# Kernel tuning notes

Measured on AMD Instinct MI355X. Metric: run time of the kernel, lower is better.

## Reference

```python
import jax, jax.numpy as jnp
import numpy as np

N_NODES = 50000
N_EDGES = 500000
NFEAT = 128
NHID = 128
NOUT = 16


def setup_inputs() -> dict:
    key = jax.random.key(0)
    ks = jax.random.split(key, 8)
    x = jax.random.normal(ks[0], (N_NODES, NFEAT), dtype=jnp.float32)
    edge_src = jax.random.randint(ks[1], (N_EDGES,), 0, N_NODES, dtype=jnp.int32)
    edge_dst = jax.random.randint(ks[2], (N_EDGES,), 0, N_NODES, dtype=jnp.int32)
    edge_weight = jax.random.uniform(ks[3], (N_EDGES,), dtype=jnp.float32)
    # Glorot-ish init for linear weights, zero bias (PyG GCNConv default bias=0)
    def glorot(k, fan_in, fan_out):
        s = jnp.sqrt(6.0 / (fan_in + fan_out))
        return jax.random.uniform(k, (fan_in, fan_out), jnp.float32, -s, s)
    W1 = glorot(ks[4], NFEAT, NHID)
    W2 = glorot(ks[5], NHID, NHID)
    W3 = glorot(ks[6], NHID, NOUT)
    b1 = jnp.zeros((NHID,), jnp.float32)
    b2 = jnp.zeros((NHID,), jnp.float32)
    b3 = jnp.zeros((NOUT,), jnp.float32)
    return {"x": x, "edge_src": edge_src, "edge_dst": edge_dst,
            "edge_weight": edge_weight, "W1": W1, "b1": b1,
            "W2": W2, "b2": b2, "W3": W3, "b3": b3}


def gcn_conv(x, src, dst, ew, W, b):
    """PyG GCNConv: symmetric-normalized aggregation with self-loops (weight 1).

    out_i = sum_{(j->i)} d_i^{-1/2} w_ji d_j^{-1/2} (x_j W) + d_i^{-1} (x_i W) + b
    where d_i = 1 + sum of incoming edge weights.
    """
    n = x.shape[0]
    xw = x @ W                                            # [N, F_out]
    deg = jax.ops.segment_sum(ew, dst, num_segments=n) + 1.0  # self-loop weight 1
    dinv = jnp.where(deg > 0, jax.lax.rsqrt(deg), 0.0)    # d^{-1/2}
    norm = dinv[src] * ew * dinv[dst]                     # [E]
    agg = jax.ops.segment_sum(xw[src] * norm[:, None], dst, num_segments=n)
    self_loop = xw * (dinv * dinv)[:, None]               # d_i^{-1} * x_i W
    return agg + self_loop + b


def reference(x, edge_src, edge_dst, edge_weight, W1, b1, W2, b2, W3, b3):
    # Dropout layers are identity in eval mode.
    h = gcn_conv(x, edge_src, edge_dst, edge_weight, W1, b1)
    h = jax.nn.relu(h)
    h = gcn_conv(h, edge_src, edge_dst, edge_weight, W2, b2)
    h = jax.nn.relu(h)
    h = gcn_conv(h, edge_src, edge_dst, edge_weight, W3, b3)
    return jax.nn.log_softmax(h, axis=1)
```

## Files before the change

### kernel.cpp

```cpp
#include <hip/hip_runtime.h>
#include <math.h>

#define NN 50000
#define NE 500000
#define NF 128
#define NO 16
#define SCAN_B 1024
#define NPART 16

typedef __attribute__((ext_vector_type(8))) _Float16 half8;


__global__ void k_count_rank(const int* __restrict__ dst, int* __restrict__ pcnt,
                             int* __restrict__ rank, int E) {
    int part = blockIdx.x & (NPART - 1);
    int e = blockIdx.x * blockDim.x + threadIdx.x;
    if (e < E) {
        int d = dst[e];
        rank[e] = atomicAdd(&pcnt[part * NN + d], 1);
    }
}

__global__ void k_combine(int* __restrict__ pcnt, int* __restrict__ counts, int N) {
    int n = blockIdx.x * blockDim.x + threadIdx.x;
    if (n < N) {
        int run = 0;
#pragma unroll
        for (int p = 0; p < NPART; ++p) {
            int v = pcnt[p * NN + n];
            pcnt[p * NN + n] = run;
            run += v;
        }
        counts[n] = run;
    }
}

__global__ void k_scan1(const int* __restrict__ counts, int* __restrict__ offs,
                        int* __restrict__ bsums, int N) {
    __shared__ int s[SCAN_B];
    int t = threadIdx.x;
    int i = blockIdx.x * SCAN_B + t;
    int c = (i < N) ? counts[i] : 0;
    s[t] = c;
    __syncthreads();
    for (int off = 1; off < SCAN_B; off <<= 1) {
        int x = (t >= off) ? s[t - off] : 0;
        __syncthreads();
        s[t] += x;
        __syncthreads();
    }
    if (i < N) offs[i] = s[t] - c;
    if (t == SCAN_B - 1) bsums[blockIdx.x] = s[t];
}

__global__ void k_scan2(int* __restrict__ bsums, int NB) {
    if (threadIdx.x == 0 && blockIdx.x == 0) {
        int run = 0;
        for (int i = 0; i < NB; ++i) { int c = bsums[i]; bsums[i] = run; run += c; }
    }
}

__global__ void k_scan3(int* __restrict__ offs, const int* __restrict__ bsums,
                        int N, int E) {
    int i = blockIdx.x * blockDim.x + threadIdx.x;
    if (i < N) {
        offs[i] = offs[i] + bsums[i >> 10];
    } else if (i == N) {
        offs[N] = E;
    }
}

__global__ void k_scatter(const int* __restrict__ src, const int* __restrict__ dst,
                          const float* __restrict__ ew, const int* __restrict__ offs,
                          const int* __restrict__ pcnt, const int* __restrict__ rank,
                          int* __restrict__ src_s, float* __restrict__ ew_s, int E) {
    int part = blockIdx.x & (NPART - 1);
    int e = blockIdx.x * blockDim.x + threadIdx.x;
    if (e < E) {
        int d = dst[e];
        int p = offs[d] + pcnt[part * NN + d] + rank[e];
        src_s[p] = src[e];
        ew_s[p]  = ew[e];
    }
}

__global__ void k_dinv_csr(const float* __restrict__ ew_s, const int* __restrict__ offs,
                           float* __restrict__ dinv, int N) {
    int n = blockIdx.x * blockDim.x + threadIdx.x;
    if (n < N) {
        float deg = 1.0f;
        int s = offs[n], e = offs[n + 1];
        for (int j = s; j < e; ++j) deg += ew_s[j];
        dinv[n] = rsqrtf(deg);
    }
}

__global__ void k_norm_csr(const float* __restrict__ ew_s, const int* __restrict__ src_s,
                           const int* __restrict__ offs, const float* __restrict__ dinv,
                           float* __restrict__ norm_s, int N) {
    int n = blockIdx.x * blockDim.x + threadIdx.x;
    if (n < N) {
        float dn = dinv[n];
        int s = offs[n], e = offs[n + 1];
        for (int j = s; j < e; ++j)
            norm_s[j] = dinv[src_s[j]] * ew_s[j] * dn;
    }
}

__global__ __launch_bounds__(256) void k_gemm128(const float* __restrict__ X,
                                                 const float* __restrict__ W,
                                                 _Float16* __restrict__ Y, int M) {
    __shared__ float Xs[64][68];
    __shared__ float Ws[64][128];
    const int tid = threadIdx.x;
    const int tx = tid & 15;
    const int ty = tid >> 4;
    const int r0g = blockIdx.x * 64;

    float acc[4][8];
#pragma unroll
    for (int i = 0; i < 4; ++i)
#pragma unroll
        for (int j = 0; j < 8; ++j) acc[i][j] = 0.0f;

    for (int kc = 0; kc < 128; kc += 64) {
        {
            int rr = tid >> 4;
            int k4 = tid & 15;
#pragma unroll
            for (int it = 0; it < 4; ++it) {
                int row = it * 16 + rr;
                int grow = r0g + row; if (grow > M - 1) grow = M - 1;
                float4 v = *(const float4*)(X + (size_t)grow * NF + kc + k4 * 4);
                *(float4*)(&Xs[row][k4 * 4]) = v;
            }
        }
        {
            int kk0 = tid >> 5;
            int c4  = tid & 31;
#pragma unroll
            for (int it = 0; it < 8; ++it) {
                int kk = it * 8 + kk0;
                float4 v = *(const float4*)(W + (size_t)(kc + kk) * NF + c4 * 4);
                *(float4*)(&Ws[kk][c4 * 4]) = v;
            }
        }
        __syncthreads();

#pragma unroll 8
        for (int k = 0; k < 64; ++k) {
            float a0 = Xs[ty * 4 + 0][k];
            float a1 = Xs[ty * 4 + 1][k];
            float a2 = Xs[ty * 4 + 2][k];
            float a3 = Xs[ty * 4 + 3][k];
            float4 b0 = *(const float4*)(&Ws[k][tx * 8]);
            float4 b1 = *(const float4*)(&Ws[k][tx * 8 + 4]);
            float bb[8] = {b0.x, b0.y, b0.z, b0.w, b1.x, b1.y, b1.z, b1.w};
#pragma unroll
            for (int j = 0; j < 8; ++j) {
                acc[0][j] = fmaf(a0, bb[j], acc[0][j]);
                acc[1][j] = fmaf(a1, bb[j], acc[1][j]);
                acc[2][j] = fmaf(a2, bb[j], acc[2][j]);
                acc[3][j] = fmaf(a3, bb[j], acc[3][j]);
            }
        }
        __syncthreads();
    }

#pragma unroll
    for (int i = 0; i < 4; ++i) {
        int row = r0g + ty * 4 + i;
        if (row < M) {
            half8 hv;
#pragma unroll
            for (int j = 0; j < 8; ++j) hv[j] = (_Float16)acc[i][j];
            *(half8*)(Y + (size_t)row * NF + tx * 8) = hv;
        }
    }
}

__global__ __launch_bounds__(256) void k_agg128h(const _Float16* __restrict__ xw,
                                                 const float* __restrict__ dinv,
                                                 const int* __restrict__ offs,
                                                 const int* __restrict__ src_s,
                                                 const float* __restrict__ norm_s,
                                                 const float* __restrict__ bias,
                                                 float* __restrict__ out, int relu) {
    const int tid = threadIdx.x;
    const int ln = tid & 63;
    int n = __builtin_amdgcn_readfirstlane(blockIdx.x * 4 + (tid >> 6));

    union CV { unsigned int u; _Float16 h[2]; };

    float di = dinv[n];
    CV sv; sv.u = *(const unsigned int*)(xw + (size_t)n * NF + ln * 2);
    float acc0 = (float)sv.h[0] * (di * di);
    float acc1 = (float)sv.h[1] * (di * di);

    int s = offs[n], e = offs[n + 1];
    int j = s;
    for (; j + 1 < e; j += 2) {
        int s0 = src_s[j], s1 = src_s[j + 1];
        float w0 = norm_s[j], w1 = norm_s[j + 1];
        CV u0, u1;
        u0.u = *(const unsigned int*)(xw + (size_t)s0 * NF + ln * 2);
        u1.u = *(const unsigned int*)(xw + (size_t)s1 * NF + ln * 2);
        acc0 = fmaf((float)u0.h[0], w0, acc0);
        acc1 = fmaf((float)u0.h[1], w0, acc1);
        acc0 = fmaf((float)u1.h[0], w1, acc0);
        acc1 = fmaf((float)u1.h[1], w1, acc1);
    }
    if (j < e) {
        int s0 = src_s[j];
        float w0 = norm_s[j];
        CV u0; u0.u = *(const unsigned int*)(xw + (size_t)s0 * NF + ln * 2);
        acc0 = fmaf((float)u0.h[0], w0, acc0);
        acc1 = fmaf((float)u0.h[1], w0, acc1);
    }
    acc0 += bias[ln * 2];
    acc1 += bias[ln * 2 + 1];
    if (relu) { acc0 = fmaxf(acc0, 0.0f); acc1 = fmaxf(acc1, 0.0f); }
    float2 o = {acc0, acc1};
    *(float2*)(out + (size_t)n * NF + ln * 2) = o;
}

__global__ __launch_bounds__(256) void k_gemm16(const float* __restrict__ H,
                                                const float* __restrict__ W3,
                                                float* __restrict__ Y, int M) {
    __shared__ float Wl[NF * NO];
    __shared__ float Hs[16 * 132];
    int tid = threadIdx.x;
    for (int i = tid; i < NF * NO; i += 256) Wl[i] = W3[i];
    int n0 = blockIdx.x * 16;
#pragma unroll
    for (int it = 0; it < 2; ++it) {
        int idx = tid + it * 256;
        int r = idx >> 5, f4 = idx & 31;
        int gr = n0 + r; if (gr > M - 1) gr = M - 1;
        *(float4*)(&Hs[r * 132 + f4 * 4]) = *(const float4*)(H + (size_t)gr * NF + f4 * 4);
    }
    __syncthreads();
    int ln = tid >> 4, c = tid & 15;
    float acc = 0.0f;
#pragma unroll 8
    for (int k = 0; k < NF; ++k) acc = fmaf(Hs[ln * 132 + k], Wl[k * NO + c], acc);
    int n = n0 + ln;
    if (n < M) Y[(size_t)n * NO + c] = acc;
}

__global__ __launch_bounds__(256) void k_agg16_ls(const float* __restrict__ xw,
                                                  const float* __restrict__ dinv,
                                                  const int* __restrict__ offs,
                                                  const int* __restrict__ src_s,
                                                  const float* __restrict__ norm_s,
                                                  const float* __restrict__ bias,
                                                  float* __restrict__ out) {
    int tid = threadIdx.x;
    int ln = tid >> 4, c = tid & 15;
    int n = blockIdx.x * 16 + ln;
    float di = dinv[n];
    float acc = xw[(size_t)n * NO + c] * (di * di);
    int s = offs[n], e = offs[n + 1];
    for (int j = s; j < e; ++j) {
        acc = fmaf(xw[(size_t)src_s[j] * NO + c], norm_s[j], acc);
    }
    acc += bias[c];
    float m = acc;
#pragma unroll
    for (int off = 8; off > 0; off >>= 1) m = fmaxf(m, __shfl_xor(m, off, 16));
    float ex = expf(acc - m);
    float ss = ex;
#pragma unroll
    for (int off = 8; off > 0; off >>= 1) ss += __shfl_xor(ss, off, 16);
    out[(size_t)n * NO + c] = acc - m - logf(ss);
}


extern "C" void kernel_launch(void* const* d_in, const int* in_sizes, int n_in,
                              void* d_out, int out_size, void* d_ws, size_t ws_size,
                              hipStream_t stream) {
    const float* x   = (const float*)d_in[0];
    const int*   esrc= (const int*)  d_in[1];
    const int*   edst= (const int*)  d_in[2];
    const float* ew  = (const float*)d_in[3];
    const float* W1  = (const float*)d_in[4];
    const float* b1  = (const float*)d_in[5];
    const float* W2  = (const float*)d_in[6];
    const float* b2  = (const float*)d_in[7];
    const float* W3  = (const float*)d_in[8];
    const float* b3  = (const float*)d_in[9];
    float* out = (float*)d_out;

    char* p = (char*)d_ws;
    _Float16* xw  = (_Float16*)p; p += (size_t)NN * NF * 2;
    float* h      = (float*)p; p += (size_t)NN * NF * 4;
    float* xw3    = (float*)p; p += (size_t)NN * NO * 4;
    float* dinv   = (float*)p; p += (size_t)NN * 4;
    float* norm_s = (float*)p; p += (size_t)NE * 4;
    int*   src_s  = (int*)p;   p += (size_t)NE * 4;
    float* ew_s   = (float*)p; p += (size_t)NE * 4;
    int*   rank   = (int*)p;   p += (size_t)NE * 4;
    int*   pcnt   = (int*)p;   p += (size_t)NPART * NN * 4;
    int*   counts = (int*)p;   p += (size_t)NN * 4;
    int*   offs   = (int*)p;   p += (size_t)(NN + 1) * 4;
    int*   bsums  = (int*)p;   p += 256;

    const int NB  = (NN + SCAN_B - 1) / SCAN_B;
    const int EBL = (NE + 255) / 256;
    const int NBL = (NN + 255) / 256;

    hipMemsetAsync(pcnt, 0, (size_t)NPART * NN * 4, stream);

    k_count_rank<<<EBL, 256, 0, stream>>>(edst, pcnt, rank, NE);
    k_combine<<<NBL, 256, 0, stream>>>(pcnt, counts, NN);
    k_scan1<<<NB, SCAN_B, 0, stream>>>(counts, offs, bsums, NN);
    k_scan2<<<1, 64, 0, stream>>>(bsums, NB);
    k_scan3<<<(NN + 256) / 256, 256, 0, stream>>>(offs, bsums, NN, NE);
    k_scatter<<<EBL, 256, 0, stream>>>(esrc, edst, ew, offs, pcnt, rank, src_s, ew_s, NE);
    k_dinv_csr<<<NBL, 256, 0, stream>>>(ew_s, offs, dinv, NN);
    k_norm_csr<<<NBL, 256, 0, stream>>>(ew_s, src_s, offs, dinv, norm_s, NN);

    k_gemm128<<<(NN + 63) / 64, 256, 0, stream>>>(x, W1, xw, NN);
    k_agg128h<<<NN / 4, 256, 0, stream>>>(xw, dinv, offs, src_s, norm_s, b1, h, 1);
    k_gemm128<<<(NN + 63) / 64, 256, 0, stream>>>(h, W2, xw, NN);
    k_agg128h<<<NN / 4, 256, 0, stream>>>(xw, dinv, offs, src_s, norm_s, b2, h, 1);
    k_gemm16<<<(NN + 15) / 16, 256, 0, stream>>>(h, W3, xw3, NN);
    k_agg16_ls<<<NN / 16, 256, 0, stream>>>(xw3, dinv, offs, src_s, norm_s, b3, out);
}
```

Before: 293.3 us.

## Use MFMA fp16 GEMMs, fold normalization into GEMM epilogue, store fp16 hidden

The scalar fp32 GEMMs are replaced by MFMA 16x16x32 fp16 kernels that read pre-transposed fp16 weights. Each kernel also pre-scales its output rows by dinv, which removes the separate per-edge norm kernel, since aggregation can then use the raw edge weights and a final dinv multiply. Hidden activations are now stored in fp16 to halve their traffic, the aggregation loop is unrolled by 4, and the block-sum scan uses a wave shuffle instead of a single thread. Lower precision in the GEMM inputs and in the hidden activations risks accuracy drift.

```diff
diff --git a/kernel.cpp b/kernel.cpp
--- a/kernel.cpp
+++ b/kernel.cpp
@@ -8,7 +8,8 @@
 #define SCAN_B 1024
 #define NPART 16
 
-typedef __attribute__((ext_vector_type(8))) _Float16 half8;
+typedef _Float16 f16x8 __attribute__((ext_vector_type(8)));
+typedef float f32x4 __attribute__((ext_vector_type(4)));
 
 
 __global__ void k_count_rank(const int* __restrict__ dst, int* __restrict__ pcnt,
@@ -54,10 +55,15 @@
 }
 
 __global__ void k_scan2(int* __restrict__ bsums, int NB) {
-    if (threadIdx.x == 0 && blockIdx.x == 0) {
-        int run = 0;
-        for (int i = 0; i < NB; ++i) { int c = bsums[i]; bsums[i] = run; run += c; }
-    }
+    int t = threadIdx.x;
+    int v = (t < NB) ? bsums[t] : 0;
+    int orig = v;
+#pragma unroll
+    for (int off = 1; off < 64; off <<= 1) {
+        int u = __shfl_up(v, off, 64);
+        if (t >= off) v += u;
+    }
+    if (t < NB) bsums[t] = v - orig;
 }
 
 __global__ void k_scan3(int* __restrict__ offs, const int* __restrict__ bsums,
@@ -95,97 +101,86 @@
     }
 }
 
-__global__ void k_norm_csr(const float* __restrict__ ew_s, const int* __restrict__ src_s,
-                           const int* __restrict__ offs, const float* __restrict__ dinv,
-                           float* __restrict__ norm_s, int N) {
-    int n = blockIdx.x * blockDim.x + threadIdx.x;
-    if (n < N) {
-        float dn = dinv[n];
-        int s = offs[n], e = offs[n + 1];
-        for (int j = s; j < e; ++j)
-            norm_s[j] = dinv[src_s[j]] * ew_s[j] * dn;
-    }
-}
-
-__global__ __launch_bounds__(256) void k_gemm128(const float* __restrict__ X,
-                                                 const float* __restrict__ W,
-                                                 _Float16* __restrict__ Y, int M) {
-    __shared__ float Xs[64][68];
-    __shared__ float Ws[64][128];
-    const int tid = threadIdx.x;
-    const int tx = tid & 15;
-    const int ty = tid >> 4;
-    const int r0g = blockIdx.x * 64;
-
-    float acc[4][8];
-#pragma unroll
-    for (int i = 0; i < 4; ++i)
-#pragma unroll
-        for (int j = 0; j < 8; ++j) acc[i][j] = 0.0f;
-
-    for (int kc = 0; kc < 128; kc += 64) {
-        {
-            int rr = tid >> 4;
-            int k4 = tid & 15;
-#pragma unroll
-            for (int it = 0; it < 4; ++it) {
-                int row = it * 16 + rr;
-                int grow = r0g + row; if (grow > M - 1) grow = M - 1;
-                float4 v = *(const float4*)(X + (size_t)grow * NF + kc + k4 * 4);
-                *(float4*)(&Xs[row][k4 * 4]) = v;
-            }
+__global__ void k_prep_w(const float* __restrict__ W1, const float* __restrict__ W2,
+                         _Float16* __restrict__ W1T, _Float16* __restrict__ W2T) {
+    int idx = blockIdx.x * 256 + threadIdx.x;
+    int r = idx >> 7, c = idx & 127;
+    W1T[(size_t)c * NF + r] = (_Float16)W1[idx];
+    W2T[(size_t)c * NF + r] = (_Float16)W2[idx];
+}
+
+
+__device__ inline f16x8 afrag_load(const float* X, int row, int k0) {
+    const float4* p = (const float4*)(X + (size_t)row * NF + k0);
+    float4 a = p[0], b = p[1];
+    f16x8 r;
+    r[0] = (_Float16)a.x; r[1] = (_Float16)a.y; r[2] = (_Float16)a.z; r[3] = (_Float16)a.w;
+    r[4] = (_Float16)b.x; r[5] = (_Float16)b.y; r[6] = (_Float16)b.z; r[7] = (_Float16)b.w;
+    return r;
+}
+__device__ inline f16x8 afrag_load(const _Float16* X, int row, int k0) {
+    return *(const f16x8*)(X + (size_t)row * NF + k0);
+}
+
+template <typename TA>
+__global__ __launch_bounds__(256) void k_gemm_mfma(const TA* __restrict__ X,
+                                                   const _Float16* __restrict__ WT,
+                                                   const float* __restrict__ dinv,
+                                                   _Float16* __restrict__ Z, int M) {
+    __shared__ _Float16 ls[4][16 * NF];
+    const int tid  = threadIdx.x;
+    const int w    = tid >> 6;
+    const int lane = tid & 63;
+    const int n16  = lane & 15;
+    const int quad = lane >> 4;
+    const int r0   = blockIdx.x * 64 + w * 16;
+
+    int arow = r0 + n16; if (arow > M - 1) arow = M - 1;
+
+    f32x4 acc[8];
+#pragma unroll
+    for (int c = 0; c < 8; ++c) acc[c] = (f32x4){0.f, 0.f, 0.f, 0.f};
+
+#pragma unroll
+    for (int kk = 0; kk < 4; ++kk) {
+        int k0 = kk * 32 + quad * 8;
+        f16x8 a = afrag_load(X, arow, k0);
+#pragma unroll
+        for (int c = 0; c < 8; ++c) {
+            f16x8 b = *(const f16x8*)(WT + (size_t)(c * 16 + n16) * NF + k0);
+            acc[c] = __builtin_amdgcn_mfma_f32_16x16x32_f16(a, b, acc[c], 0, 0, 0);
         }
-        {
-            int kk0 = tid >> 5;
-            int c4  = tid & 31;
-#pragma unroll
-            for (int it = 0; it < 8; ++it) {
-                int kk = it * 8 + kk0;
-                float4 v = *(const float4*)(W + (size_t)(kc + kk) * NF + c4 * 4);
-                *(float4*)(&Ws[kk][c4 * 4]) = v;
-            }
+    }
+
+#pragma unroll
+    for (int reg = 0; reg < 4; ++reg) {
+        int lrow = quad * 4 + reg;
+        int grow = r0 + lrow; if (grow > M - 1) grow = M - 1;
+        float di = dinv[grow];
+#pragma unroll
+        for (int c = 0; c < 8; ++c)
+            ls[w][lrow * NF + c * 16 + n16] = (_Float16)(acc[c][reg] * di);
+    }
+    __syncthreads();
+#pragma unroll
+    for (int i = 0; i < 4; ++i) {
+        int off16 = i * 64 + lane;
+        int row = off16 >> 4;
+        int grow = r0 + row;
+        if (grow < M) {
+            f16x8 v = *(const f16x8*)(&ls[w][off16 * 8]);
+            *(f16x8*)(Z + (size_t)grow * NF + (off16 & 15) * 8) = v;
         }
-        __syncthreads();
-
-#pragma unroll 8
-        for (int k = 0; k < 64; ++k) {
-            float a0 = Xs[ty * 4 + 0][k];
-            float a1 = Xs[ty * 4 + 1][k];
-            float a2 = Xs[ty * 4 + 2][k];
-            float a3 = Xs[ty * 4 + 3][k];
-            float4 b0 = *(const float4*)(&Ws[k][tx * 8]);
-            float4 b1 = *(const float4*)(&Ws[k][tx * 8 + 4]);
-            float bb[8] = {b0.x, b0.y, b0.z, b0.w, b1.x, b1.y, b1.z, b1.w};
-#pragma unroll
-            for (int j = 0; j < 8; ++j) {
-                acc[0][j] = fmaf(a0, bb[j], acc[0][j]);
-                acc[1][j] = fmaf(a1, bb[j], acc[1][j]);
-                acc[2][j] = fmaf(a2, bb[j], acc[2][j]);
-                acc[3][j] = fmaf(a3, bb[j], acc[3][j]);
-            }
-        }
-        __syncthreads();
-    }
-
-#pragma unroll
-    for (int i = 0; i < 4; ++i) {
-        int row = r0g + ty * 4 + i;
-        if (row < M) {
-            half8 hv;
-#pragma unroll
-            for (int j = 0; j < 8; ++j) hv[j] = (_Float16)acc[i][j];
-            *(half8*)(Y + (size_t)row * NF + tx * 8) = hv;
-        }
-    }
-}
-
-__global__ __launch_bounds__(256) void k_agg128h(const _Float16* __restrict__ xw,
+    }
+}
+
+__global__ __launch_bounds__(256) void k_agg128h(const _Float16* __restrict__ z,
                                                  const float* __restrict__ dinv,
                                                  const int* __restrict__ offs,
                                                  const int* __restrict__ src_s,
-                                                 const float* __restrict__ norm_s,
+                                                 const float* __restrict__ ew_s,
                                                  const float* __restrict__ bias,
-                                                 float* __restrict__ out, int relu) {
+                                                 _Float16* __restrict__ hout, int relu) {
     const int tid = threadIdx.x;
     const int ln = tid & 63;
     int n = __builtin_amdgcn_readfirstlane(blockIdx.x * 4 + (tid >> 6));
@@ -193,51 +188,57 @@
     union CV { unsigned int u; _Float16 h[2]; };
 
     float di = dinv[n];
-    CV sv; sv.u = *(const unsigned int*)(xw + (size_t)n * NF + ln * 2);
-    float acc0 = (float)sv.h[0] * (di * di);
-    float acc1 = (float)sv.h[1] * (di * di);
+    CV sv; sv.u = *(const unsigned int*)(z + (size_t)n * NF + ln * 2);
+    float acc0 = (float)sv.h[0];
+    float acc1 = (float)sv.h[1];
 
     int s = offs[n], e = offs[n + 1];
     int j = s;
-    for (; j + 1 < e; j += 2) {
-        int s0 = src_s[j], s1 = src_s[j + 1];
-        float w0 = norm_s[j], w1 = norm_s[j + 1];
-        CV u0, u1;
-        u0.u = *(const unsigned int*)(xw + (size_t)s0 * NF + ln * 2);
-        u1.u = *(const unsigned int*)(xw + (size_t)s1 * NF + ln * 2);
+    for (; j + 3 < e; j += 4) {
+        int s0 = src_s[j], s1 = src_s[j + 1], s2 = src_s[j + 2], s3 = src_s[j + 3];
+        float w0 = ew_s[j], w1 = ew_s[j + 1], w2 = ew_s[j + 2], w3 = ew_s[j + 3];
+        CV u0, u1, u2, u3;
+        u0.u = *(const unsigned int*)(z + (size_t)s0 * NF + ln * 2);
+        u1.u = *(const unsigned int*)(z + (size_t)s1 * NF + ln * 2);
+        u2.u = *(const unsigned int*)(z + (size_t)s2 * NF + ln * 2);
+        u3.u = *(const unsigned int*)(z + (size_t)s3 * NF + ln * 2);
+        acc0 = fmaf((float)u0.h[0], w0, acc0); acc1 = fmaf((float)u0.h[1], w0, acc1);
+        acc0 = fmaf((float)u1.h[0], w1, acc0); acc1 = fmaf((float)u1.h[1], w1, acc1);
+        acc0 = fmaf((float)u2.h[0], w2, acc0); acc1 = fmaf((float)u2.h[1], w2, acc1);
+        acc0 = fmaf((float)u3.h[0], w3, acc0); acc1 = fmaf((float)u3.h[1], w3, acc1);
+    }
+    for (; j < e; ++j) {
+        int s0 = src_s[j];
+        float w0 = ew_s[j];
+        CV u0; u0.u = *(const unsigned int*)(z + (size_t)s0 * NF + ln * 2);
         acc0 = fmaf((float)u0.h[0], w0, acc0);
         acc1 = fmaf((float)u0.h[1], w0, acc1);
-        acc0 = fmaf((float)u1.h[0], w1, acc0);
-        acc1 = fmaf((float)u1.h[1], w1, acc1);
-    }
-    if (j < e) {
-        int s0 = src_s[j];
-        float w0 = norm_s[j];
-        CV u0; u0.u = *(const unsigned int*)(xw + (size_t)s0 * NF + ln * 2);
-        acc0 = fmaf((float)u0.h[0], w0, acc0);
-        acc1 = fmaf((float)u0.h[1], w0, acc1);
-    }
-    acc0 += bias[ln * 2];
-    acc1 += bias[ln * 2 + 1];
+    }
+    float2 bb = *(const float2*)(bias + ln * 2);
+    acc0 = fmaf(di, acc0, bb.x);
+    acc1 = fmaf(di, acc1, bb.y);
     if (relu) { acc0 = fmaxf(acc0, 0.0f); acc1 = fmaxf(acc1, 0.0f); }
-    float2 o = {acc0, acc1};
-    *(float2*)(out + (size_t)n * NF + ln * 2) = o;
-}
-
-__global__ __launch_bounds__(256) void k_gemm16(const float* __restrict__ H,
+    CV o; o.h[0] = (_Float16)acc0; o.h[1] = (_Float16)acc1;
+    *(unsigned int*)(hout + (size_t)n * NF + ln * 2) = o.u;
+}
+
+__global__ __launch_bounds__(256) void k_gemm16(const _Float16* __restrict__ H,
                                                 const float* __restrict__ W3,
-                                                float* __restrict__ Y, int M) {
+                                                const float* __restrict__ dinv,
+                                                float* __restrict__ Z3, int M) {
     __shared__ float Wl[NF * NO];
     __shared__ float Hs[16 * 132];
     int tid = threadIdx.x;
     for (int i = tid; i < NF * NO; i += 256) Wl[i] = W3[i];
     int n0 = blockIdx.x * 16;
-#pragma unroll
-    for (int it = 0; it < 2; ++it) {
-        int idx = tid + it * 256;
-        int r = idx >> 5, f4 = idx & 31;
-        int gr = n0 + r; if (gr > M - 1) gr = M - 1;
-        *(float4*)(&Hs[r * 132 + f4 * 4]) = *(const float4*)(H + (size_t)gr * NF + f4 * 4);
+    {
+        int row = tid >> 4, h8 = tid & 15;
+        int gr = n0 + row; if (gr > M - 1) gr = M - 1;
+        f16x8 v = *(const f16x8*)(H + (size_t)gr * NF + h8 * 8);
+        float4 f0 = {(float)v[0], (float)v[1], (float)v[2], (float)v[3]};
+        float4 f1 = {(float)v[4], (float)v[5], (float)v[6], (float)v[7]};
+        *(float4*)(&Hs[row * 132 + h8 * 8])     = f0;
+        *(float4*)(&Hs[row * 132 + h8 * 8 + 4]) = f1;
     }
     __syncthreads();
     int ln = tid >> 4, c = tid & 15;
@@ -245,26 +246,25 @@
 #pragma unroll 8
     for (int k = 0; k < NF; ++k) acc = fmaf(Hs[ln * 132 + k], Wl[k * NO + c], acc);
     int n = n0 + ln;
-    if (n < M) Y[(size_t)n * NO + c] = acc;
-}
-
-__global__ __launch_bounds__(256) void k_agg16_ls(const float* __restrict__ xw,
+    if (n < M) Z3[(size_t)n * NO + c] = acc * dinv[n];
+}
+
+__global__ __launch_bounds__(256) void k_agg16_ls(const float* __restrict__ z3,
                                                   const float* __restrict__ dinv,
                                                   const int* __restrict__ offs,
                                                   const int* __restrict__ src_s,
-                                                  const float* __restrict__ norm_s,
+                                                  const float* __restrict__ ew_s,
                                                   const float* __restrict__ bias,
                                                   float* __restrict__ out) {
     int tid = threadIdx.x;
     int ln = tid >> 4, c = tid & 15;
     int n = blockIdx.x * 16 + ln;
-    float di = dinv[n];
-    float acc = xw[(size_t)n * NO + c] * (di * di);
+    float acc = z3[(size_t)n * NO + c];
     int s = offs[n], e = offs[n + 1];
     for (int j = s; j < e; ++j) {
-        acc = fmaf(xw[(size_t)src_s[j] * NO + c], norm_s[j], acc);
-    }
-    acc += bias[c];
+        acc = fmaf(z3[(size_t)src_s[j] * NO + c], ew_s[j], acc);
+    }
+    acc = fmaf(dinv[n], acc, bias[c]);
     float m = acc;
 #pragma unroll
     for (int off = 8; off > 0; off >>= 1) m = fmaxf(m, __shfl_xor(m, off, 16));
@@ -292,18 +292,19 @@
     float* out = (float*)d_out;
 
     char* p = (char*)d_ws;
-    _Float16* xw  = (_Float16*)p; p += (size_t)NN * NF * 2;
-    float* h      = (float*)p; p += (size_t)NN * NF * 4;
-    float* xw3    = (float*)p; p += (size_t)NN * NO * 4;
+    _Float16* z   = (_Float16*)p; p += (size_t)NN * NF * 2;
+    _Float16* h   = (_Float16*)p; p += (size_t)NN * NF * 2;
+    float* z3     = (float*)p; p += (size_t)NN * NO * 4;
     float* dinv   = (float*)p; p += (size_t)NN * 4;
-    float* norm_s = (float*)p; p += (size_t)NE * 4;
+    float* ew_s   = (float*)p; p += (size_t)NE * 4;
     int*   src_s  = (int*)p;   p += (size_t)NE * 4;
-    float* ew_s   = (float*)p; p += (size_t)NE * 4;
     int*   rank   = (int*)p;   p += (size_t)NE * 4;
     int*   pcnt   = (int*)p;   p += (size_t)NPART * NN * 4;
     int*   counts = (int*)p;   p += (size_t)NN * 4;
     int*   offs   = (int*)p;   p += (size_t)(NN + 1) * 4;
     int*   bsums  = (int*)p;   p += 256;
+    _Float16* W1T = (_Float16*)p; p += (size_t)NF * NF * 2;
+    _Float16* W2T = (_Float16*)p; p += (size_t)NF * NF * 2;
 
     const int NB  = (NN + SCAN_B - 1) / SCAN_B;
     const int EBL = (NE + 255) / 256;
@@ -318,12 +319,12 @@
     k_scan3<<<(NN + 256) / 256, 256, 0, stream>>>(offs, bsums, NN, NE);
     k_scatter<<<EBL, 256, 0, stream>>>(esrc, edst, ew, offs, pcnt, rank, src_s, ew_s, NE);
     k_dinv_csr<<<NBL, 256, 0, stream>>>(ew_s, offs, dinv, NN);
-    k_norm_csr<<<NBL, 256, 0, stream>>>(ew_s, src_s, offs, dinv, norm_s, NN);
-
-    k_gemm128<<<(NN + 63) / 64, 256, 0, stream>>>(x, W1, xw, NN);
-    k_agg128h<<<NN / 4, 256, 0, stream>>>(xw, dinv, offs, src_s, norm_s, b1, h, 1);
-    k_gemm128<<<(NN + 63) / 64, 256, 0, stream>>>(h, W2, xw, NN);
-    k_agg128h<<<NN / 4, 256, 0, stream>>>(xw, dinv, offs, src_s, norm_s, b2, h, 1);
-    k_gemm16<<<(NN + 15) / 16, 256, 0, stream>>>(h, W3, xw3, NN);
-    k_agg16_ls<<<NN / 16, 256, 0, stream>>>(xw3, dinv, offs, src_s, norm_s, b3, out);
-}
+    k_prep_w<<<64, 256, 0, stream>>>(W1, W2, W1T, W2T);
+
+    k_gemm_mfma<float><<<(NN + 63) / 64, 256, 0, stream>>>(x, W1T, dinv, z, NN);
+    k_agg128h<<<NN / 4, 256, 0, stream>>>(z, dinv, offs, src_s, ew_s, b1, h, 1);
+    k_gemm_mfma<_Float16><<<(NN + 63) / 64, 256, 0, stream>>>(h, W2T, dinv, z, NN);
+    k_agg128h<<<NN / 4, 256, 0, stream>>>(z, dinv, offs, src_s, ew_s, b2, h, 1);
+    k_gemm16<<<(NN + 15) / 16, 256, 0, stream>>>(h, W3, dinv, z3, NN);
+    k_agg16_ls<<<NN / 16, 256, 0, stream>>>(z3, dinv, offs, src_s, ew_s, b3, out);
+}
```

Result: faster. 266.7 us (-9.1%).
